# Kernel tuning notes

Hardware: AMD Instinct MI355X
Metric: run time of the kernel (lower is better)

The kernel has to match this reference:

```python
import jax, jax.numpy as jnp
import numpy as np

B, T, D = 16, 512, 256          # batch, seq_len, d_model (= num features = num graph nodes N)
H, MC, K, DE, DH = 4, 4, 3, 10, 128
GS, SS, AS = 4, 6, 4            # global/sector/asset regime states
TAU = 0.5
STEPS = 3                       # diffusion steps
HID = max(64, D)
DEC_H = max(64, D // 2)


def setup_inputs() -> dict:
    key = jax.random.key(0)
    ks = iter(jax.random.split(key, 64))

    def nrm(shape, s=0.02):
        return (s * jax.random.normal(next(ks), shape)).astype(jnp.float32)

    z = lambda *s: jnp.zeros(s, jnp.float32)
    o = lambda *s: jnp.ones(s, jnp.float32)
    p = dict(
        x=jax.random.normal(next(ks), (B, T, D), dtype=jnp.float32),
        # hierarchical regime controller
        gW1=nrm((D, HID)), gb1=z(HID), g_ln_w=o(HID), g_ln_b=z(HID),
        gW2=nrm((HID, GS)), gb2=z(GS),
        sW1=nrm((D, HID)), sb1=z(HID), sW2=nrm((HID, D * SS)), sb2=z(D * SS),
        aW1=nrm((D, HID)), ab1=z(HID), aW2=nrm((HID, D * AS)), ab2=z(D * AS),
        global_prior=z(GS), sector_prior=z(SS), asset_prior=z(AS),
        g2f=nrm((GS, D)),
        sector_emb=jax.random.normal(next(ks), (SS, D), dtype=jnp.float32),
        asset_emb=jax.random.normal(next(ks), (AS, D), dtype=jnp.float32),
        # bidirectional temporal scan (BI-Mamba stand-in)
        decay_f=nrm((D,), 1.0), decay_b=nrm((D,), 1.0),
        tW=nrm((D, D)), tb=z(D),
        # Bayesian MAGAC + diffusion graph prior
        psi=nrm((H, D, DE), 0.1), log_sigma=jnp.full((H,), -2.0, jnp.float32),
        step_logits=jnp.linspace(-1.0, 0.5, STEPS).astype(jnp.float32),
        noise_scale=jnp.full((STEPS,), 0.05, jnp.float32),
        Wk=nrm((K + 1, T, DH)),
        mean_w=nrm((DH,)), mean_b=z(), lv_w=nrm((DH,)), lv_b=z(),
        # risk-aware decoder
        dW1=nrm((D, DEC_H)), db1=z(DEC_H), d_ln_w=o(DEC_H), d_ln_b=z(DEC_H),
        mW=nrm((DEC_H,)), mb=z(), lvW=nrm((DEC_H,)), lvb=z(),
        cW=nrm((DEC_H,)), cb=z(),
    )
    return p


def _ln(h, w, b):
    m = h.mean(-1, keepdims=True)
    v = h.var(-1, keepdims=True)  # biased, matches torch LayerNorm
    return (h - m) / jnp.sqrt(v + 1e-5) * w + b


def _gelu(h):
    return jax.nn.gelu(h, approximate=False)


def _gumbel_softmax(k, logits):
    u = jax.random.uniform(k, logits.shape, minval=1e-6, maxval=1.0 - 1e-6)
    g = -jnp.log(-jnp.log(u))
    return jax.nn.softmax((logits + g) / TAU, axis=-1)


def _fwd(x, gW1, gb1, g_ln_w, g_ln_b, gW2, gb2, sW1, sb1, sW2, sb2,
         aW1, ab1, aW2, ab2, global_prior, sector_prior, asset_prior,
         g2f, sector_emb, asset_emb, decay_f, decay_b, tW, tb,
         psi, log_sigma, step_logits, noise_scale, Wk,
         mean_w, mean_b, lv_w, lv_b,
         dW1, db1, d_ln_w, d_ln_b, mW, mb, lvW, lvb, cW, cb):
    rk = jax.random.key(42)
    k_g, k_s, k_a, k_eps, k_diff = jax.random.split(rk, 5)

    # ---- hierarchical regime controller ----
    seq_mean = x.mean(1)                               # (B, D)
    diff_summary = (x[:, 1:] - x[:, :-1]).mean(1)      # (B, D)
    g_logits = _gelu(_ln(seq_mean @ gW1 + gb1, g_ln_w, g_ln_b)) @ gW2 + gb2
    s_logits = (_gelu(seq_mean @ sW1 + sb1) @ sW2 + sb2).reshape(B, D, SS)
    a_logits = (_gelu(diff_summary @ aW1 + ab1) @ aW2 + ab2).reshape(B, D, AS)
    g_probs = _gumbel_softmax(k_g, g_logits)
    s_probs = _gumbel_softmax(k_s, s_logits)
    a_probs = _gumbel_softmax(k_a, a_logits)
    global_gate = g_probs @ g2f                                   # (B, D)
    # diagonal of einsum('bfs,sd->bfd') == einsum('bfs,sf->bf')
    sector_gate = jnp.einsum('bfs,sf->bf', s_probs, sector_emb)
    asset_gate = jnp.einsum('bfs,sf->bf', a_probs, asset_emb)
    feature_gate = jax.nn.sigmoid(global_gate + sector_gate + asset_gate)
    gated_x = x * feature_gate[:, None, :]

    # ---- bidirectional temporal EMA scan (BI-Mamba stand-in) ----
    af = jax.nn.sigmoid(decay_f)
    abk = jax.nn.sigmoid(decay_b)
    xs = gated_x.transpose(1, 0, 2)                    # (T, B, D)

    def ema(a):
        def step(h, xt):
            h = a * h + (1.0 - a) * xt
            return h, h
        return step

    _, hf = jax.lax.scan(ema(af), jnp.zeros_like(xs[0]), xs)
    _, hb = jax.lax.scan(ema(abk), jnp.zeros_like(xs[0]), xs[::-1])
    temporal = (hf + hb[::-1]).transpose(1, 0, 2) @ tW + tb       # (B, T, D)
    node_major = temporal.transpose(0, 2, 1)                      # (B, N=D, T)

    # ---- Bayesian adjacency sampling (MC samples per head) ----
    logits = jnp.einsum('hne,hme->hnm', psi, psi) / jnp.sqrt(jnp.float32(DE))
    sigma = jnp.exp(log_sigma)                                    # (H,)
    eps = jax.random.normal(k_eps, (MC, H, D, D))
    A = jax.nn.softmax(logits[None] + sigma[None, :, None, None] * eps, axis=-1)

    # ---- diffusion refinement guided by regime features ----
    ctx = feature_gate.mean(0)
    ctx = ctx / (jnp.linalg.norm(ctx) + 1e-6)
    outer = ctx[:, None] * ctx[None, :]
    outer = outer / jnp.maximum(outer.sum(-1, keepdims=True), 1e-6)
    dkeys = jax.random.split(k_diff, STEPS)
    for s in range(STEPS):                             # fixed small loop, vectorized over (MC,H)
        alpha = jax.nn.sigmoid(step_logits[s])
        noise = noise_scale[s] * jax.random.normal(dkeys[s], A.shape)
        A = alpha * A + (1.0 - alpha) * outer + noise
        A = 0.5 * (A + jnp.swapaxes(A, -1, -2))
        A = jax.nn.softmax(A, axis=-1)

    # ---- K-hop graph conv, averaged over MC samples and heads ----
    Z = jnp.einsum('bnt,td->bnd', node_major, Wk[0])[None, None]  # hop 0
    P = jnp.broadcast_to(node_major, (MC, H, B, D, T))
    for k in range(1, K + 1):
        P = jnp.einsum('mhnp,mhbpt->mhbnt', A, P)
        Z = Z + jnp.einsum('mhbnt,td->mhbnd', P, Wk[k])
    Z = Z.mean((0, 1))                                            # (B, N, DH)
    graph_mean = Z @ mean_w + mean_b                              # (B, N)
    graph_logvar = Z @ lv_w + lv_b                                # (B, N)

    # ---- risk-aware decoder ----
    feat = _ln(_gelu(graph_mean @ dW1 + db1), d_ln_w, d_ln_b)     # (B, DEC_H)
    mean = feat @ mW + mb
    dec_logvar = feat @ lvW + lvb
    _cvar = jax.nn.sigmoid(feat @ cW + cb)  # auxiliary head (not in returned output)
    var = jnp.exp(dec_logvar) + jnp.exp(graph_logvar).sum(1)
    log_var = jnp.log(var)
    return jnp.stack([mean, log_var], axis=-1)                    # (B, 2)


def reference(x, gW1, gb1, g_ln_w, g_ln_b, gW2, gb2, sW1, sb1, sW2, sb2,
              aW1, ab1, aW2, ab2, global_prior, sector_prior, asset_prior,
              g2f, sector_emb, asset_emb, decay_f, decay_b, tW, tb,
              psi, log_sigma, step_logits, noise_scale, Wk,
              mean_w, mean_b, lv_w, lv_b,
              dW1, db1, d_ln_w, d_ln_b, mW, mb, lvW, lvb, cW, cb):
    return _fwd(x, gW1, gb1, g_ln_w, g_ln_b, gW2, gb2, sW1, sb1, sW2, sb2,
                aW1, ab1, aW2, ab2, global_prior, sector_prior, asset_prior,
                g2f, sector_emb, asset_emb, decay_f, decay_b, tW, tb,
                psi, log_sigma, step_logits, noise_scale, Wk,
                mean_w, mean_b, lv_w, lv_b,
                dW1, db1, d_ln_w, d_ln_b, mW, mb, lvW, lvb, cW, cb)
```

## Files before the change

### kernel.cpp

```cpp
#include <hip/hip_runtime.h>
#include <stdint.h>

#define PARTITIONABLE 1

namespace {

struct TFPair { uint32_t a, b; };

__host__ __device__ constexpr uint32_t rotl32(uint32_t x, int d) {
  return (x << d) | (x >> (32 - d));
}

__host__ __device__ constexpr TFPair tf2x32(uint32_t k0, uint32_t k1,
                                            uint32_t x0, uint32_t x1) {
  uint32_t k2 = k0 ^ k1 ^ 0x1BD11BDAu;
  x0 += k0; x1 += k1;
  x0 += x1; x1 = rotl32(x1, 13); x1 ^= x0;
  x0 += x1; x1 = rotl32(x1, 15); x1 ^= x0;
  x0 += x1; x1 = rotl32(x1, 26); x1 ^= x0;
  x0 += x1; x1 = rotl32(x1, 6);  x1 ^= x0;
  x0 += k1; x1 += k2 + 1u;
  x0 += x1; x1 = rotl32(x1, 17); x1 ^= x0;
  x0 += x1; x1 = rotl32(x1, 29); x1 ^= x0;
  x0 += x1; x1 = rotl32(x1, 16); x1 ^= x0;
  x0 += x1; x1 = rotl32(x1, 24); x1 ^= x0;
  x0 += k2; x1 += k0 + 2u;
  x0 += x1; x1 = rotl32(x1, 13); x1 ^= x0;
  x0 += x1; x1 = rotl32(x1, 15); x1 ^= x0;
  x0 += x1; x1 = rotl32(x1, 26); x1 ^= x0;
  x0 += x1; x1 = rotl32(x1, 6);  x1 ^= x0;
  x0 += k0; x1 += k1 + 3u;
  x0 += x1; x1 = rotl32(x1, 17); x1 ^= x0;
  x0 += x1; x1 = rotl32(x1, 29); x1 ^= x0;
  x0 += x1; x1 = rotl32(x1, 16); x1 ^= x0;
  x0 += x1; x1 = rotl32(x1, 24); x1 ^= x0;
  x0 += k1; x1 += k2 + 4u;
  x0 += x1; x1 = rotl32(x1, 13); x1 ^= x0;
  x0 += x1; x1 = rotl32(x1, 15); x1 ^= x0;
  x0 += x1; x1 = rotl32(x1, 26); x1 ^= x0;
  x0 += x1; x1 = rotl32(x1, 6);  x1 ^= x0;
  x0 += k2; x1 += k0 + 5u;
  return TFPair{x0, x1};
}

#if PARTITIONABLE
constexpr TFPair KG  = tf2x32(0u, 42u, 0u, 0u);
constexpr TFPair KS  = tf2x32(0u, 42u, 0u, 1u);
constexpr TFPair KA  = tf2x32(0u, 42u, 0u, 2u);
constexpr TFPair KE  = tf2x32(0u, 42u, 0u, 3u);
constexpr TFPair KD  = tf2x32(0u, 42u, 0u, 4u);
constexpr TFPair DK0 = tf2x32(KD.a, KD.b, 0u, 0u);
constexpr TFPair DK1 = tf2x32(KD.a, KD.b, 0u, 1u);
constexpr TFPair DK2 = tf2x32(KD.a, KD.b, 0u, 2u);
#else
constexpr TFPair SP0 = tf2x32(0u, 42u, 0u, 5u);
constexpr TFPair SP1 = tf2x32(0u, 42u, 1u, 6u);
constexpr TFPair SP2 = tf2x32(0u, 42u, 2u, 7u);
constexpr TFPair SP3 = tf2x32(0u, 42u, 3u, 8u);
constexpr TFPair SP4 = tf2x32(0u, 42u, 4u, 9u);
constexpr TFPair KG  = TFPair{SP0.a, SP1.a};
constexpr TFPair KS  = TFPair{SP2.a, SP3.a};
constexpr TFPair KA  = TFPair{SP4.a, SP0.b};
constexpr TFPair KE  = TFPair{SP1.b, SP2.b};
constexpr TFPair KD  = TFPair{SP3.b, SP4.b};
constexpr TFPair DP0 = tf2x32(KD.a, KD.b, 0u, 3u);
constexpr TFPair DP1 = tf2x32(KD.a, KD.b, 1u, 4u);
constexpr TFPair DP2 = tf2x32(KD.a, KD.b, 2u, 5u);
constexpr TFPair DK0 = TFPair{DP0.a, DP1.a};
constexpr TFPair DK1 = TFPair{DP2.a, DP0.b};
constexpr TFPair DK2 = TFPair{DP1.b, DP2.b};
#endif

__device__ __forceinline__ uint32_t rbits(uint32_t k0, uint32_t k1,
                                          uint32_t idx, uint32_t half) {
#if PARTITIONABLE
  TFPair t = tf2x32(k0, k1, 0u, idx);
  return t.a ^ t.b;
#else
  if (idx < half) return tf2x32(k0, k1, idx, idx + half).a;
  return tf2x32(k0, k1, idx - half, idx).b;
#endif
}

__device__ __forceinline__ float bits_to_u01(uint32_t bits) {
  return __uint_as_float((bits >> 9) | 0x3F800000u) - 1.0f;
}

__device__ __forceinline__ float gumbel_u(uint32_t k0, uint32_t k1,
                                          uint32_t idx, uint32_t half) {
  const float mn = 1e-6f;
  const float mx = 1.0f - 1e-6f;
  float f = bits_to_u01(rbits(k0, k1, idx, half));
  return fmaxf(mn, f * (mx - mn) + mn);
}

__device__ __forceinline__ float erfinv_f32(float x) {
  float w = -log1pf(-x * x);
  float p;
  if (w < 5.0f) {
    w -= 2.5f;
    p = 2.81022636e-08f;
    p = fmaf(p, w, 3.43273939e-07f);
    p = fmaf(p, w, -3.5233877e-06f);
    p = fmaf(p, w, -4.39150654e-06f);
    p = fmaf(p, w, 0.00021858087f);
    p = fmaf(p, w, -0.00125372503f);
    p = fmaf(p, w, -0.00417768164f);
    p = fmaf(p, w, 0.246640727f);
    p = fmaf(p, w, 1.50140941f);
  } else {
    w = sqrtf(w) - 3.0f;
    p = -0.000200214257f;
    p = fmaf(p, w, 0.000100950558f);
    p = fmaf(p, w, 0.00134934322f);
    p = fmaf(p, w, -0.00367342844f);
    p = fmaf(p, w, 0.00573950773f);
    p = fmaf(p, w, -0.0076224613f);
    p = fmaf(p, w, 0.00943887047f);
    p = fmaf(p, w, 1.00167406f);
    p = fmaf(p, w, 2.83297682f);
  }
  return p * x;
}

__device__ __forceinline__ float normal_from(uint32_t k0, uint32_t k1,
                                             uint32_t idx, uint32_t half) {
  const float lo = -0x1.fffffep-1f;
  float f = bits_to_u01(rbits(k0, k1, idx, half));
  float u = fmaxf(lo, f * 2.0f + lo);
  return 1.41421356237f * erfinv_f32(u);
}

__device__ __forceinline__ float gelu_f(float x) {
  return 0.5f * x * (1.0f + erff(x / 1.4142135623730951f));
}
__device__ __forceinline__ float sigmoid_f(float x) {
  return 1.0f / (1.0f + expf(-x));
}

__device__ __forceinline__ float wave_sum(float v) {
  #pragma unroll
  for (int m = 32; m > 0; m >>= 1) v += __shfl_xor(v, m);
  return v;
}
__device__ __forceinline__ float wave_max(float v) {
  #pragma unroll
  for (int m = 32; m > 0; m >>= 1) v = fmaxf(v, __shfl_xor(v, m));
  return v;
}
template <int NW>
__device__ __forceinline__ float blk_sum(float v, float* slots) {
  v = wave_sum(v);
  int wid = threadIdx.x >> 6;
  if ((threadIdx.x & 63) == 0) slots[wid] = v;
  __syncthreads();
  float r = slots[0];
  #pragma unroll
  for (int i = 1; i < NW; ++i) r += slots[i];
  return r;
}
template <int NW>
__device__ __forceinline__ float blk_max(float v, float* slots) {
  v = wave_max(v);
  int wid = threadIdx.x >> 6;
  if ((threadIdx.x & 63) == 0) slots[wid] = v;
  __syncthreads();
  float r = slots[0];
  #pragma unroll
  for (int i = 1; i < NW; ++i) r = fmaxf(r, slots[i]);
  return r;
}

struct Params {
  const float *x, *gW1, *gb1, *glnw, *glnb, *gW2, *gb2, *sW1, *sb1, *sW2, *sb2,
      *aW1, *ab1, *aW2, *ab2, *g2f, *semb, *aemb, *decay_f, *decay_b, *tW, *tb,
      *psi, *log_sigma, *step_logits, *noise_scale, *Wk, *mean_w, *mean_b,
      *lv_w, *lv_b, *dW1, *db1, *dlnw, *dlnb, *mW, *mb, *lvW, *lvb;
  float* out;
  float *ps, *ds, *fg, *ctx, *v, *sv, *u, *Pf, *Qf, *Pb, *Qb, *Lf, *Lb, *YH,
      *R1, *R2, *gm, *glv, *A, *A2, *nz;
};


__device__ __forceinline__ void phase_xsum(const Params& P, int bid, int tid) {
  int b = bid >> 4, tc = bid & 15;
  const float* xp = P.x + ((size_t)b * 512 + tc * 32) * 256 + tid;
  float s = 0.f;
  for (int i = 0; i < 32; ++i) s += xp[(size_t)i * 256];
  P.ps[(size_t)bid * 256 + tid] = s;
  if (tc == 0) {
    const float* xb = P.x + (size_t)b * 512 * 256 + tid;
    P.ds[b * 256 + tid] = (xb[(size_t)511 * 256] - xb[0]) / 511.0f;
  }
}

__device__ __forceinline__ void phase_ainit_row(const Params& P, float* smem,
                                                int blk, int tid) {
  float* pn = smem;
  float* s1 = smem + 12;
  float* s2 = smem + 16;
  int mh = blk >> 8, h = mh & 3, n = blk & 255, p = tid;
  if (p < 10) pn[p] = P.psi[(size_t)(h * 256 + n) * 10 + p];
  __syncthreads();
  const float* pp = P.psi + (size_t)(h * 256 + p) * 10;
  float s = 0.f;
  #pragma unroll
  for (int e = 0; e < 10; ++e) s = fmaf(pn[e], pp[e], s);
  float logit = s / sqrtf(10.0f);
  uint32_t idx = (uint32_t)blk * 256u + (uint32_t)p;
  float eps = normal_from(KE.a, KE.b, idx, 524288u);
  float val = logit + expf(P.log_sigma[h]) * eps;
  float mx = blk_max<4>(val, s1);
  float e = expf(val - mx);
  float sum = blk_sum<4>(e, s2);
  P.A[(size_t)blk * 256 + p] = e / sum;
}

__device__ __forceinline__ void phase_noise(const Params& P, int blk2,
                                            int tid) {
  const uint32_t dka[3] = {DK0.a, DK1.a, DK2.a};
  const uint32_t dkb[3] = {DK0.b, DK1.b, DK2.b};
  int s = blk2 >> 12;
  int row = blk2 & 4095;
  uint32_t e = (uint32_t)row * 256u + (uint32_t)tid;
  float z = normal_from(dka[s], dkb[s], e, 524288u);
  P.nz[(size_t)s * 1048576 + e] = P.noise_scale[s] * z;
}

__device__ __forceinline__ void phase_vcompute(const Params& P, int bid2,
                                               int tid) {
  int j = bid2 >> 2, tg = bid2 & 3;
  const float* wp = (j & 1) ? P.lv_w : P.mean_w;
  const float* Wkk = P.Wk + (size_t)(j >> 1) * 65536;
  int wid = tid >> 6, lane = tid & 63;
  float w0 = wp[lane], w1 = wp[64 + lane];
  for (int i = 0; i < 32; ++i) {
    int t = tg * 128 + wid * 32 + i;
    const float* row = Wkk + (size_t)t * 128;
    float s = row[lane] * w0 + row[64 + lane] * w1;
    s = wave_sum(s);
    if (lane == 0) P.v[j * 512 + t] = s;
  }
}

__device__ __forceinline__ void phase_svsum(const Params& P, float* smem,
                                            int tid) {
  float* slots = smem;
  #pragma unroll
  for (int j = 0; j < 8; ++j) {
    float val = P.v[j * 512 + tid] + P.v[j * 512 + 256 + tid];
    float s = blk_sum<4>(val, slots + 4 * j);
    if (tid == 0) P.sv[j] = s;
    __syncthreads();
  }
}

__device__ __forceinline__ void phase_hidden_gates(const Params& P,
                                                   float* smem, int bid,
                                                   int tid) {
  float* sms = smem;
  float* dss = smem + 256;
  float* hgG = smem + 512;
  float* hgS = smem + 768;
  float* hgA = smem + 1024;
  float* lvS = smem + 1280;
  float* lvA = smem + 1664;
  float* gsl = smem + 1920;
  float* gvals = smem + 1936;
  float* gpv = smem + 1940;
  float* s1 = smem + 1944;
  float* s2 = smem + 1948;
  int b = bid >> 2, f0 = (bid & 3) * 64;
  {
    float s = 0.f;
    for (int tc = 0; tc < 16; ++tc)
      s += P.ps[(size_t)(b * 16 + tc) * 256 + tid];
    sms[tid] = s / 512.0f;
    dss[tid] = P.ds[b * 256 + tid];
  }
  __syncthreads();
  {
    float h = P.gb1[tid];
    for (int d = 0; d < 256; ++d) h = fmaf(sms[d], P.gW1[d * 256 + tid], h);
    float mean = blk_sum<4>(h, s1) / 256.0f;
    float dv = h - mean;
    float var = blk_sum<4>(dv * dv, s2) / 256.0f;
    h = dv / sqrtf(var + 1e-5f) * P.glnw[tid] + P.glnb[tid];
    hgG[tid] = gelu_f(h);
    float h2 = P.sb1[tid];
    for (int d = 0; d < 256; ++d) h2 = fmaf(sms[d], P.sW1[d * 256 + tid], h2);
    hgS[tid] = gelu_f(h2);
    float h3 = P.ab1[tid];
    for (int d = 0; d < 256; ++d) h3 = fmaf(dss[d], P.aW1[d * 256 + tid], h3);
    hgA[tid] = gelu_f(h3);
  }
  __syncthreads();
  float lg[4];
  #pragma unroll
  for (int s = 0; s < 4; ++s)
    lg[s] = blk_sum<4>(hgG[tid] * P.gW2[tid * 4 + s], gsl + 4 * s);
  if (tid < 4) {
    float u = gumbel_u(KG.a, KG.b, (uint32_t)(b * 4 + tid), 32u);
    float g = -logf(-logf(u));
    gvals[tid] = (lg[tid] + P.gb2[tid] + g) / 0.5f;
  }
  __syncthreads();
  if (tid < 4) {
    float mx = fmaxf(fmaxf(gvals[0], gvals[1]), fmaxf(gvals[2], gvals[3]));
    float sum = expf(gvals[0] - mx) + expf(gvals[1] - mx) +
                expf(gvals[2] - mx) + expf(gvals[3] - mx);
    gpv[tid] = expf(gvals[tid] - mx) / sum;
  }
  {
    int o = tid;
    int fl = o / 6, s = o - fl * 6;
    int f = f0 + fl;
    const float* wp = P.sW2 + f * 6 + s;
    float acc = P.sb2[f * 6 + s];
    for (int d = 0; d < 256; ++d) acc = fmaf(hgS[d], wp[(size_t)d * 1536], acc);
    float u = gumbel_u(KS.a, KS.b, (uint32_t)(b * 256 + f) * 6u + s, 12288u);
    lvS[o] = (acc + (-logf(-logf(u)))) / 0.5f;
  }
  if (tid < 128) {
    int o = tid + 256;
    int fl = o / 6, s = o - fl * 6;
    int f = f0 + fl;
    const float* wp = P.sW2 + f * 6 + s;
    float acc = P.sb2[f * 6 + s];
    for (int d = 0; d < 256; ++d) acc = fmaf(hgS[d], wp[(size_t)d * 1536], acc);
    float u = gumbel_u(KS.a, KS.b, (uint32_t)(b * 256 + f) * 6u + s, 12288u);
    lvS[o] = (acc + (-logf(-logf(u)))) / 0.5f;
  }
  {
    int fl = tid >> 2, s = tid & 3;
    int f = f0 + fl;
    const float* wp = P.aW2 + f * 4 + s;
    float acc = P.ab2[f * 4 + s];
    for (int d = 0; d < 256; ++d) acc = fmaf(hgA[d], wp[(size_t)d * 1024], acc);
    float u = gumbel_u(KA.a, KA.b, (uint32_t)(b * 256 + f) * 4u + s, 8192u);
    lvA[tid] = (acc + (-logf(-logf(u)))) / 0.5f;
  }
  __syncthreads();
  if (tid < 64) {
    int f = f0 + tid;
    float v0 = lvS[tid * 6 + 0], v1 = lvS[tid * 6 + 1], v2 = lvS[tid * 6 + 2];
    float v3 = lvS[tid * 6 + 3], v4 = lvS[tid * 6 + 4], v5 = lvS[tid * 6 + 5];
    float mx = fmaxf(fmaxf(fmaxf(v0, v1), fmaxf(v2, v3)), fmaxf(v4, v5));
    float e0 = expf(v0 - mx), e1 = expf(v1 - mx), e2 = expf(v2 - mx);
    float e3 = expf(v3 - mx), e4 = expf(v4 - mx), e5 = expf(v5 - mx);
    float ssum = e0 + e1 + e2 + e3 + e4 + e5;
    float sg = (e0 / ssum) * P.semb[0 * 256 + f] + (e1 / ssum) * P.semb[1 * 256 + f] +
               (e2 / ssum) * P.semb[2 * 256 + f] + (e3 / ssum) * P.semb[3 * 256 + f] +
               (e4 / ssum) * P.semb[4 * 256 + f] + (e5 / ssum) * P.semb[5 * 256 + f];
    float a0 = lvA[tid * 4 + 0], a1 = lvA[tid * 4 + 1];
    float a2 = lvA[tid * 4 + 2], a3 = lvA[tid * 4 + 3];
    float amx = fmaxf(fmaxf(a0, a1), fmaxf(a2, a3));
    float x0 = expf(a0 - amx), x1 = expf(a1 - amx);
    float x2 = expf(a2 - amx), x3 = expf(a3 - amx);
    float asum = x0 + x1 + x2 + x3;
    float ag = (x0 / asum) * P.aemb[0 * 256 + f] + (x1 / asum) * P.aemb[1 * 256 + f] +
               (x2 / asum) * P.aemb[2 * 256 + f] + (x3 / asum) * P.aemb[3 * 256 + f];
    float gg = 0.f;
    #pragma unroll
    for (int s = 0; s < 4; ++s) gg = fmaf(gpv[s], P.g2f[s * 256 + f], gg);
    P.fg[b * 256 + f] = sigmoid_f(gg + sg + ag);
  }
}

__device__ __forceinline__ void phase_scan1(const Params& P, float* smem,
                                            int ch, int tid) {
  float* vv = smem;
  int b = ch >> 4, c = ch & 15;
  int d = tid;
  vv[(d >> 5) * 32 + (d & 31)] = P.v[(d >> 5) * 512 + c * 32 + (d & 31)];
  __syncthreads();
  float af = sigmoid_f(P.decay_f[d]);
  float ab = sigmoid_f(P.decay_b[d]);
  float r_x[32];
  const float* xp = P.x + ((size_t)b * 512 + c * 32) * 256 + d;
  #pragma unroll
  for (int i = 0; i < 32; ++i) r_x[i] = xp[(size_t)i * 256];
  float h = 0.f, pw = 1.f;
  float Pr[8], Q[8];
  #pragma unroll
  for (int j = 0; j < 8; ++j) { Pr[j] = 0.f; Q[j] = 0.f; }
  #pragma unroll
  for (int i = 0; i < 32; ++i) {
    h = fmaf(af, h, (1.0f - af) * r_x[i]);
    pw *= af;
    #pragma unroll
    for (int j = 0; j < 8; ++j) {
      float vj = vv[j * 32 + i];
      Pr[j] = fmaf(h, vj, Pr[j]);
      Q[j] = fmaf(pw, vj, Q[j]);
    }
  }
  size_t base = ((size_t)(b * 16 + c) * 8) * 256 + d;
  #pragma unroll
  for (int j = 0; j < 8; ++j) {
    P.Pf[base + j * 256] = Pr[j];
    P.Qf[base + j * 256] = Q[j];
  }
  P.Lf[(b * 16 + c) * 256 + d] = h;
  h = 0.f; pw = 1.f;
  #pragma unroll
  for (int j = 0; j < 8; ++j) { Pr[j] = 0.f; Q[j] = 0.f; }
  #pragma unroll
  for (int i = 31; i >= 0; --i) {
    h = fmaf(ab, h, (1.0f - ab) * r_x[i]);
    pw *= ab;
    #pragma unroll
    for (int j = 0; j < 8; ++j) {
      float vj = vv[j * 32 + i];
      Pr[j] = fmaf(h, vj, Pr[j]);
      Q[j] = fmaf(pw, vj, Q[j]);
    }
  }
  #pragma unroll
  for (int j = 0; j < 8; ++j) {
    P.Pb[base + j * 256] = Pr[j];
    P.Qb[base + j * 256] = Q[j];
  }
  P.Lb[(b * 16 + c) * 256 + d] = h;
}

__device__ __forceinline__ void phase_scan2(const Params& P, int blk, int tid) {
  int b = blk >> 3, j = blk & 7;
  int d = tid;
  float af = sigmoid_f(P.decay_f[d]);
  float ab = sigmoid_f(P.decay_b[d]);
  float af32 = af, ab32 = ab;
  #pragma unroll
  for (int q = 0; q < 5; ++q) { af32 *= af32; ab32 *= ab32; }
  float acc = 0.f, H = 0.f;
  for (int c = 0; c < 16; ++c) {
    size_t base = ((size_t)(b * 16 + c) * 8 + j) * 256 + d;
    acc += P.Pf[base] + H * P.Qf[base];
    H = P.Lf[(b * 16 + c) * 256 + d] + af32 * H;
  }
  H = 0.f;
  for (int c = 15; c >= 0; --c) {
    size_t base = ((size_t)(b * 16 + c) * 8 + j) * 256 + d;
    acc += P.Pb[base] + H * P.Qb[base];
    H = P.Lb[(b * 16 + c) * 256 + d] + ab32 * H;
  }
  P.u[(b * 8 + j) * 256 + d] = acc;
}

__device__ __forceinline__ void phase_ctx(const Params& P, float* smem,
                                          int tid) {
  float* s1 = smem;
  float* s2 = smem + 4;
  float c = 0.f;
  for (int b = 0; b < 16; ++b) c += P.fg[b * 256 + tid];
  c /= 16.0f;
  float ss = blk_sum<4>(c * c, s1);
  float cv = c / (sqrtf(ss) + 1e-6f);
  P.ctx[tid] = cv;
  float S = blk_sum<4>(cv, s2);
  if (tid == 0) P.ctx[256] = S;
}

__device__ __forceinline__ void phase_ygemm(const Params& P, float* smem,
                                            int blk32, int tid) {
  float* As = smem;
  float* Bs = smem + 1056;
  float* svs = smem + 2112;
  int n0 = (blk32 & 7) * 32, m0 = (blk32 >> 3) * 32;
  int tx = tid & 31, ty = tid >> 5;
  if (tid < 8) svs[tid] = P.sv[tid];
  float acc[4] = {0.f, 0.f, 0.f, 0.f};
  for (int k0 = 0; k0 < 256; k0 += 32) {
    #pragma unroll
    for (int l = 0; l < 4; ++l) {
      int e = tid + l * 256, r = e >> 5, cc = e & 31;
      int row = m0 + r;
      As[r * 33 + cc] = P.u[(size_t)row * 256 + k0 + cc] *
                        P.fg[(row >> 3) * 256 + k0 + cc];
      Bs[r * 33 + cc] = P.tW[(size_t)(k0 + r) * 256 + n0 + cc];
    }
    __syncthreads();
    #pragma unroll
    for (int kk = 0; kk < 32; ++kk) {
      float bv = Bs[kk * 33 + tx];
      #pragma unroll
      for (int i = 0; i < 4; ++i)
        acc[i] = fmaf(As[(ty + 8 * i) * 33 + kk], bv, acc[i]);
    }
    __syncthreads();
  }
  int n = n0 + tx;
  float tbn = P.tb[n];
  float mb0 = P.mean_b[0], lb0 = P.lv_b[0];
  #pragma unroll
  for (int i = 0; i < 4; ++i) {
    int row = m0 + ty + 8 * i;
    int b = row >> 3, j = row & 7;
    float val = acc[i] + tbn * svs[j];
    if (j == 0) P.gm[b * 256 + n] = val + mb0;
    else if (j == 1) P.glv[b * 256 + n] = val + lb0;
    else {
      int k = (j >> 1) - 1, proj = j & 1;
      P.YH[k * 8192 + n * 32 + b * 2 + proj] = val;
    }
  }
}

__device__ __forceinline__ void phase_mix_row(const Params& P, float* smem,
                                              int sidx, const float* Ain,
                                              float* Aout, int blk, int tid) {
  float* s1 = smem;
  float* s2 = smem + 4;
  float alpha = sigmoid_f(P.step_logits[sidx]);
  float S = P.ctx[256];
  float cp = P.ctx[tid];
  int mh = blk >> 8, n = blk & 255, p = tid;
  float cn = P.ctx[n];
  float o_np = (cn * cp) / fmaxf(cn * S, 1e-6f);
  float o_pn = (cp * cn) / fmaxf(cp * S, 1e-6f);
  const float* nzs = P.nz + (size_t)sidx * 1048576;
  float nz_np = nzs[(size_t)blk * 256 + p];
  float nz_pn = nzs[(size_t)mh * 65536 + (size_t)p * 256 + n];
  float a_np = Ain[(size_t)mh * 65536 + n * 256 + p];
  float a_pn = Ain[(size_t)mh * 65536 + p * 256 + n];
  float m_np = alpha * a_np + (1.0f - alpha) * o_np + nz_np;
  float m_pn = alpha * a_pn + (1.0f - alpha) * o_pn + nz_pn;
  float val = 0.5f * (m_np + m_pn);
  float mx = blk_max<4>(val, s1);
  float e = expf(val - mx);
  float sum = blk_sum<4>(e, s2);
  Aout[(size_t)blk * 256 + p] = e / sum;
}

__device__ __forceinline__ void phase_horner(const Params& P, float* smem,
                                             const float* A, const float* Rin,
                                             int sRin, const float* Yadd,
                                             float* Rout, int bid, int tid) {
  float* As = smem;
  float* Bs = smem + 1056;
  int nt = bid & 7, mh = bid >> 3;
  int n0 = nt * 32;
  int tx = tid & 31, ty = tid >> 5;
  float acc[4] = {0.f, 0.f, 0.f, 0.f};
  const float* Ab = A + (size_t)mh * 65536;
  const float* Rb = Rin + (size_t)mh * sRin;
  for (int k0 = 0; k0 < 256; k0 += 32) {
    #pragma unroll
    for (int l = 0; l < 4; ++l) {
      int e = tid + l * 256, r = e >> 5, cc = e & 31;
      As[r * 33 + cc] = Ab[(size_t)(n0 + r) * 256 + k0 + cc];
      Bs[r * 33 + cc] = Rb[(size_t)(k0 + r) * 32 + cc];
    }
    __syncthreads();
    #pragma unroll
    for (int kk = 0; kk < 32; ++kk) {
      float bv = Bs[kk * 33 + tx];
      #pragma unroll
      for (int i = 0; i < 4; ++i)
        acc[i] = fmaf(As[(ty + 8 * i) * 33 + kk], bv, acc[i]);
    }
    __syncthreads();
  }
  #pragma unroll
  for (int i = 0; i < 4; ++i) {
    int n = n0 + ty + 8 * i;
    float vv = acc[i];
    if (Yadd) vv += Yadd[n * 32 + tx];
    Rout[(size_t)mh * 8192 + (size_t)n * 32 + tx] = vv;
  }
}

__device__ __forceinline__ void phase_horner_final(const Params& P,
                                                   float* smem, int bid,
                                                   int tid) {
  float* As = smem;
  float* Bs = smem + 1056;
  int nt = bid & 7, mh = bid >> 3;
  int n0 = nt * 32;
  int tx = tid & 31, ty = tid >> 5;
  float acc[4] = {0.f, 0.f, 0.f, 0.f};
  const float* Ab = P.A2 + (size_t)mh * 65536;
  const float* Rb = P.R2 + (size_t)mh * 8192;
  for (int k0 = 0; k0 < 256; k0 += 32) {
    #pragma unroll
    for (int l = 0; l < 4; ++l) {
      int e = tid + l * 256, r = e >> 5, cc = e & 31;
      As[r * 33 + cc] = Ab[(size_t)(n0 + r) * 256 + k0 + cc];
      Bs[r * 33 + cc] = Rb[(size_t)(k0 + r) * 32 + cc];
    }
    __syncthreads();
    #pragma unroll
    for (int kk = 0; kk < 32; ++kk) {
      float bv = Bs[kk * 33 + tx];
      #pragma unroll
      for (int i = 0; i < 4; ++i)
        acc[i] = fmaf(As[(ty + 8 * i) * 33 + kk], bv, acc[i]);
    }
    __syncthreads();
  }
  int bb = tx >> 1, proj = tx & 1;
  float* dst = proj ? P.glv : P.gm;
  #pragma unroll
  for (int i = 0; i < 4; ++i) {
    int n = n0 + ty + 8 * i;
    atomicAdd(dst + bb * 256 + n, acc[i] * 0.0625f);
  }
}

__device__ __forceinline__ void phase_findec(const Params& P, float* smem,
                                             int bid, int tid) {
  float* gmv = smem;
  float* sl = smem + 256;
  int b = bid;
  float gmn = P.gm[b * 256 + tid];
  float gln = P.glv[b * 256 + tid];
  gmv[tid] = gmn;
  float se = expf(gln);
  __syncthreads();
  float sumexp = blk_sum<4>(se, sl);
  float h = 0.f;
  if (tid < 128) {
    h = P.db1[tid];
    for (int n = 0; n < 256; ++n) h = fmaf(gmv[n], P.dW1[n * 128 + tid], h);
    h = gelu_f(h);
  }
  float mean = blk_sum<4>(tid < 128 ? h : 0.f, sl + 4) / 128.0f;
  float dv = (tid < 128) ? h - mean : 0.f;
  float var = blk_sum<4>(dv * dv, sl + 8) / 128.0f;
  float feat = (tid < 128) ? dv / sqrtf(var + 1e-5f) * P.dlnw[tid] + P.dlnb[tid]
                           : 0.f;
  float m_c = blk_sum<4>(tid < 128 ? feat * P.mW[tid] : 0.f, sl + 12) + P.mb[0];
  float lv_c = blk_sum<4>(tid < 128 ? feat * P.lvW[tid] : 0.f, sl + 16) + P.lvb[0];
  if (tid == 0) {
    P.out[b * 2 + 0] = m_c;
    P.out[b * 2 + 1] = logf(expf(lv_c) + sumexp);
  }
}


__global__ __launch_bounds__(256) void kN0(Params P) {
  __shared__ float smem[20];
  int bid = blockIdx.x, tid = threadIdx.x;
  if (bid < 256) phase_xsum(P, bid, tid);
  else if (bid < 4352) phase_ainit_row(P, smem, bid - 256, tid);
  else if (bid < 16640) phase_noise(P, bid - 4352, tid);
  else phase_vcompute(P, bid - 16640, tid);
}

__global__ __launch_bounds__(256) void kN1(Params P) {
  __shared__ float smem[1952];
  int bid = blockIdx.x, tid = threadIdx.x;
  if (bid < 64) phase_hidden_gates(P, smem, bid, tid);
  else if (bid < 320) phase_scan1(P, smem, bid - 64, tid);
  else phase_svsum(P, smem, tid);
}

__global__ __launch_bounds__(256) void kN2(Params P) {
  __shared__ float smem[8];
  int bid = blockIdx.x, tid = threadIdx.x;
  if (bid < 128) phase_scan2(P, bid, tid);
  else phase_ctx(P, smem, tid);
}

__global__ __launch_bounds__(256) void kM0(Params P) {
  __shared__ float smem[2120];
  int bid = blockIdx.x, tid = threadIdx.x;
  if (bid < 4096) phase_mix_row(P, smem, 0, P.A, P.A2, bid, tid);
  else phase_ygemm(P, smem, bid - 4096, tid);
}
__global__ __launch_bounds__(256) void kM1(Params P) {
  __shared__ float smem[8];
  phase_mix_row(P, smem, 1, P.A2, P.A, blockIdx.x, threadIdx.x);
}
__global__ __launch_bounds__(256) void kM2(Params P) {
  __shared__ float smem[8];
  phase_mix_row(P, smem, 2, P.A, P.A2, blockIdx.x, threadIdx.x);
}

__global__ __launch_bounds__(256) void kH1(Params P) {
  __shared__ float smem[2112];
  phase_horner(P, smem, P.A2, P.YH + 2 * 8192, 0, P.YH + 8192, P.R1,
               blockIdx.x, threadIdx.x);
}
__global__ __launch_bounds__(256) void kH2(Params P) {
  __shared__ float smem[2112];
  phase_horner(P, smem, P.A2, P.R1, 8192, P.YH, P.R2, blockIdx.x, threadIdx.x);
}
__global__ __launch_bounds__(256) void kH3(Params P) {
  __shared__ float smem[2112];
  phase_horner_final(P, smem, blockIdx.x, threadIdx.x);
}

__global__ __launch_bounds__(256) void kFin(Params P) {
  __shared__ float smem[276];
  phase_findec(P, smem, blockIdx.x, threadIdx.x);
}

constexpr size_t O_PS = 0;
constexpr size_t O_DS = 65536;
constexpr size_t O_FG = 69632;
constexpr size_t O_CTX = 73728;
constexpr size_t O_V = 74048;
constexpr size_t O_SV = 78144;
constexpr size_t O_U = 78208;
constexpr size_t O_PF = 110976;
constexpr size_t O_QF = 635264;
constexpr size_t O_PB = 1159552;
constexpr size_t O_QB = 1683840;
constexpr size_t O_LF = 2208128;
constexpr size_t O_LB = 2273664;
constexpr size_t O_YH = 2339200;
constexpr size_t O_R1 = 2363776;
constexpr size_t O_R2 = 2494848;
constexpr size_t O_GM = 2625920;
constexpr size_t O_GLV = 2630016;
constexpr size_t O_A = 2634112;
constexpr size_t O_A2 = 3682688;
constexpr size_t O_NZ = 4731264;

}

extern "C" void kernel_launch(void* const* d_in, const int* in_sizes, int n_in,
                              void* d_out, int out_size, void* d_ws,
                              size_t ws_size, hipStream_t stream) {
  (void)in_sizes; (void)n_in; (void)out_size; (void)ws_size;
  float* w = (float*)d_ws;
  Params prm;
  prm.x = (const float*)d_in[0];
  prm.gW1 = (const float*)d_in[1];
  prm.gb1 = (const float*)d_in[2];
  prm.glnw = (const float*)d_in[3];
  prm.glnb = (const float*)d_in[4];
  prm.gW2 = (const float*)d_in[5];
  prm.gb2 = (const float*)d_in[6];
  prm.sW1 = (const float*)d_in[7];
  prm.sb1 = (const float*)d_in[8];
  prm.sW2 = (const float*)d_in[9];
  prm.sb2 = (const float*)d_in[10];
  prm.aW1 = (const float*)d_in[11];
  prm.ab1 = (const float*)d_in[12];
  prm.aW2 = (const float*)d_in[13];
  prm.ab2 = (const float*)d_in[14];
  prm.g2f = (const float*)d_in[18];
  prm.semb = (const float*)d_in[19];
  prm.aemb = (const float*)d_in[20];
  prm.decay_f = (const float*)d_in[21];
  prm.decay_b = (const float*)d_in[22];
  prm.tW = (const float*)d_in[23];
  prm.tb = (const float*)d_in[24];
  prm.psi = (const float*)d_in[25];
  prm.log_sigma = (const float*)d_in[26];
  prm.step_logits = (const float*)d_in[27];
  prm.noise_scale = (const float*)d_in[28];
  prm.Wk = (const float*)d_in[29];
  prm.mean_w = (const float*)d_in[30];
  prm.mean_b = (const float*)d_in[31];
  prm.lv_w = (const float*)d_in[32];
  prm.lv_b = (const float*)d_in[33];
  prm.dW1 = (const float*)d_in[34];
  prm.db1 = (const float*)d_in[35];
  prm.dlnw = (const float*)d_in[36];
  prm.dlnb = (const float*)d_in[37];
  prm.mW = (const float*)d_in[38];
  prm.mb = (const float*)d_in[39];
  prm.lvW = (const float*)d_in[40];
  prm.lvb = (const float*)d_in[41];
  prm.out = (float*)d_out;
  prm.ps = w + O_PS;
  prm.ds = w + O_DS;
  prm.fg = w + O_FG;
  prm.ctx = w + O_CTX;
  prm.v = w + O_V;
  prm.sv = w + O_SV;
  prm.u = w + O_U;
  prm.Pf = w + O_PF;
  prm.Qf = w + O_QF;
  prm.Pb = w + O_PB;
  prm.Qb = w + O_QB;
  prm.Lf = w + O_LF;
  prm.Lb = w + O_LB;
  prm.YH = w + O_YH;
  prm.R1 = w + O_R1;
  prm.R2 = w + O_R2;
  prm.gm = w + O_GM;
  prm.glv = w + O_GLV;
  prm.A = w + O_A;
  prm.A2 = w + O_A2;
  prm.nz = w + O_NZ;

  kN0<<<16672, 256, 0, stream>>>(prm);
  kN1<<<321, 256, 0, stream>>>(prm);
  kN2<<<129, 256, 0, stream>>>(prm);
  kM0<<<4128, 256, 0, stream>>>(prm);
  kM1<<<4096, 256, 0, stream>>>(prm);
  kM2<<<4096, 256, 0, stream>>>(prm);
  kH1<<<128, 256, 0, stream>>>(prm);
  kH2<<<128, 256, 0, stream>>>(prm);
  kH3<<<128, 256, 0, stream>>>(prm);
  kFin<<<16, 256, 0, stream>>>(prm);
}
```

Before: 344.3 us.

## Split hidden-layer GEMVs from gate computation and rebalance kernel stages

The first-layer controller GEMVs move out of the per-(batch, feature-quarter) gate blocks into a separate phase with one block per (head, batch). Each hidden vector is now computed once instead of four times, and the work is spread over 48 blocks instead of being serialized inside 64. The gate logic moves to the next kernel and reads the hidden vectors from workspace. ygemm and ctx move to a new small kernel, so kM0 becomes a pure mix kernel, at the cost of one extra launch and extra workspace traffic.

```diff
diff --git a/kernel.cpp b/kernel.cpp
--- a/kernel.cpp
+++ b/kernel.cpp
@@ -177,8 +177,8 @@
       *psi, *log_sigma, *step_logits, *noise_scale, *Wk, *mean_w, *mean_b,
       *lv_w, *lv_b, *dW1, *db1, *dlnw, *dlnb, *mW, *mb, *lvW, *lvb;
   float* out;
-  float *ps, *ds, *fg, *ctx, *v, *sv, *u, *Pf, *Qf, *Pb, *Qb, *Lf, *Lb, *YH,
-      *R1, *R2, *gm, *glv, *A, *A2, *nz;
+  float *ps, *ds, *hgG, *hgS, *hgA, *fg, *ctx, *v, *sv, *u, *Pf, *Qf, *Pb,
+      *Qb, *Lf, *Lb, *YH, *R1, *R2, *gm, *glv, *A, *A2, *nz;
 };
 
 
@@ -243,6 +243,37 @@
   }
 }
 
+__device__ __forceinline__ void phase_hidden(const Params& P, float* smem,
+                                             int bid, int tid) {
+  float* inv = smem;
+  float* s1 = smem + 256;
+  float* s2 = smem + 260;
+  int head = bid >> 4, b = bid & 15;
+  float iv;
+  if (head < 2) {
+    float s = 0.f;
+    for (int tc = 0; tc < 16; ++tc)
+      s += P.ps[(size_t)(b * 16 + tc) * 256 + tid];
+    iv = s / 512.0f;
+  } else {
+    iv = P.ds[b * 256 + tid];
+  }
+  inv[tid] = iv;
+  __syncthreads();
+  const float* W1 = (head == 0) ? P.gW1 : (head == 1) ? P.sW1 : P.aW1;
+  const float* b1 = (head == 0) ? P.gb1 : (head == 1) ? P.sb1 : P.ab1;
+  float h = b1[tid];
+  for (int d = 0; d < 256; ++d) h = fmaf(inv[d], W1[d * 256 + tid], h);
+  if (head == 0) {
+    float mean = blk_sum<4>(h, s1) / 256.0f;
+    float dv = h - mean;
+    float var = blk_sum<4>(dv * dv, s2) / 256.0f;
+    h = dv / sqrtf(var + 1e-5f) * P.glnw[tid] + P.glnb[tid];
+  }
+  float* outp = (head == 0) ? P.hgG : (head == 1) ? P.hgS : P.hgA;
+  outp[b * 256 + tid] = gelu_f(h);
+}
+
 __device__ __forceinline__ void phase_svsum(const Params& P, float* smem,
                                             int tid) {
   float* slots = smem;
@@ -255,50 +286,25 @@
   }
 }
 
-__device__ __forceinline__ void phase_hidden_gates(const Params& P,
-                                                   float* smem, int bid,
-                                                   int tid) {
-  float* sms = smem;
-  float* dss = smem + 256;
-  float* hgG = smem + 512;
-  float* hgS = smem + 768;
-  float* hgA = smem + 1024;
-  float* lvS = smem + 1280;
-  float* lvA = smem + 1664;
-  float* gsl = smem + 1920;
-  float* gvals = smem + 1936;
-  float* gpv = smem + 1940;
-  float* s1 = smem + 1944;
-  float* s2 = smem + 1948;
+__device__ __forceinline__ void phase_gates(const Params& P, float* smem,
+                                            int bid, int tid) {
+  float* hgGs = smem;
+  float* hgSs = smem + 256;
+  float* hgAs = smem + 512;
+  float* lvS = smem + 768;
+  float* lvA = smem + 1152;
+  float* gsl = smem + 1408;
+  float* gvals = smem + 1424;
+  float* gpv = smem + 1428;
   int b = bid >> 2, f0 = (bid & 3) * 64;
-  {
-    float s = 0.f;
-    for (int tc = 0; tc < 16; ++tc)
-      s += P.ps[(size_t)(b * 16 + tc) * 256 + tid];
-    sms[tid] = s / 512.0f;
-    dss[tid] = P.ds[b * 256 + tid];
-  }
-  __syncthreads();
-  {
-    float h = P.gb1[tid];
-    for (int d = 0; d < 256; ++d) h = fmaf(sms[d], P.gW1[d * 256 + tid], h);
-    float mean = blk_sum<4>(h, s1) / 256.0f;
-    float dv = h - mean;
-    float var = blk_sum<4>(dv * dv, s2) / 256.0f;
-    h = dv / sqrtf(var + 1e-5f) * P.glnw[tid] + P.glnb[tid];
-    hgG[tid] = gelu_f(h);
-    float h2 = P.sb1[tid];
-    for (int d = 0; d < 256; ++d) h2 = fmaf(sms[d], P.sW1[d * 256 + tid], h2);
-    hgS[tid] = gelu_f(h2);
-    float h3 = P.ab1[tid];
-    for (int d = 0; d < 256; ++d) h3 = fmaf(dss[d], P.aW1[d * 256 + tid], h3);
-    hgA[tid] = gelu_f(h3);
-  }
+  hgGs[tid] = P.hgG[b * 256 + tid];
+  hgSs[tid] = P.hgS[b * 256 + tid];
+  hgAs[tid] = P.hgA[b * 256 + tid];
   __syncthreads();
   float lg[4];
   #pragma unroll
   for (int s = 0; s < 4; ++s)
-    lg[s] = blk_sum<4>(hgG[tid] * P.gW2[tid * 4 + s], gsl + 4 * s);
+    lg[s] = blk_sum<4>(hgGs[tid] * P.gW2[tid * 4 + s], gsl + 4 * s);
   if (tid < 4) {
     float u = gumbel_u(KG.a, KG.b, (uint32_t)(b * 4 + tid), 32u);
     float g = -logf(-logf(u));
@@ -317,7 +323,7 @@
     int f = f0 + fl;
     const float* wp = P.sW2 + f * 6 + s;
     float acc = P.sb2[f * 6 + s];
-    for (int d = 0; d < 256; ++d) acc = fmaf(hgS[d], wp[(size_t)d * 1536], acc);
+    for (int d = 0; d < 256; ++d) acc = fmaf(hgSs[d], wp[(size_t)d * 1536], acc);
     float u = gumbel_u(KS.a, KS.b, (uint32_t)(b * 256 + f) * 6u + s, 12288u);
     lvS[o] = (acc + (-logf(-logf(u)))) / 0.5f;
   }
@@ -327,7 +333,7 @@
     int f = f0 + fl;
     const float* wp = P.sW2 + f * 6 + s;
     float acc = P.sb2[f * 6 + s];
-    for (int d = 0; d < 256; ++d) acc = fmaf(hgS[d], wp[(size_t)d * 1536], acc);
+    for (int d = 0; d < 256; ++d) acc = fmaf(hgSs[d], wp[(size_t)d * 1536], acc);
     float u = gumbel_u(KS.a, KS.b, (uint32_t)(b * 256 + f) * 6u + s, 12288u);
     lvS[o] = (acc + (-logf(-logf(u)))) / 0.5f;
   }
@@ -336,7 +342,7 @@
     int f = f0 + fl;
     const float* wp = P.aW2 + f * 4 + s;
     float acc = P.ab2[f * 4 + s];
-    for (int d = 0; d < 256; ++d) acc = fmaf(hgA[d], wp[(size_t)d * 1024], acc);
+    for (int d = 0; d < 256; ++d) acc = fmaf(hgAs[d], wp[(size_t)d * 1024], acc);
     float u = gumbel_u(KA.a, KA.b, (uint32_t)(b * 256 + f) * 4u + s, 8192u);
     lvA[tid] = (acc + (-logf(-logf(u)))) / 0.5f;
   }
@@ -648,25 +654,30 @@
 }
 
 __global__ __launch_bounds__(256) void kN1(Params P) {
-  __shared__ float smem[1952];
+  __shared__ float smem[264];
   int bid = blockIdx.x, tid = threadIdx.x;
-  if (bid < 64) phase_hidden_gates(P, smem, bid, tid);
-  else if (bid < 320) phase_scan1(P, smem, bid - 64, tid);
+  if (bid < 48) phase_hidden(P, smem, bid, tid);
+  else if (bid < 304) phase_scan1(P, smem, bid - 48, tid);
   else phase_svsum(P, smem, tid);
 }
 
 __global__ __launch_bounds__(256) void kN2(Params P) {
-  __shared__ float smem[8];
+  __shared__ float smem[1440];
   int bid = blockIdx.x, tid = threadIdx.x;
-  if (bid < 128) phase_scan2(P, bid, tid);
-  else phase_ctx(P, smem, tid);
-}
-
-__global__ __launch_bounds__(256) void kM0(Params P) {
+  if (bid < 64) phase_gates(P, smem, bid, tid);
+  else phase_scan2(P, bid - 64, tid);
+}
+
+__global__ __launch_bounds__(256) void kN3(Params P) {
   __shared__ float smem[2120];
   int bid = blockIdx.x, tid = threadIdx.x;
-  if (bid < 4096) phase_mix_row(P, smem, 0, P.A, P.A2, bid, tid);
-  else phase_ygemm(P, smem, bid - 4096, tid);
+  if (bid < 32) phase_ygemm(P, smem, bid, tid);
+  else phase_ctx(P, smem, tid);
+}
+
+__global__ __launch_bounds__(256) void kM0(Params P) {
+  __shared__ float smem[8];
+  phase_mix_row(P, smem, 0, P.A, P.A2, blockIdx.x, threadIdx.x);
 }
 __global__ __launch_bounds__(256) void kM1(Params P) {
   __shared__ float smem[8];
@@ -698,25 +709,28 @@
 
 constexpr size_t O_PS = 0;
 constexpr size_t O_DS = 65536;
-constexpr size_t O_FG = 69632;
-constexpr size_t O_CTX = 73728;
-constexpr size_t O_V = 74048;
-constexpr size_t O_SV = 78144;
-constexpr size_t O_U = 78208;
-constexpr size_t O_PF = 110976;
-constexpr size_t O_QF = 635264;
-constexpr size_t O_PB = 1159552;
-constexpr size_t O_QB = 1683840;
-constexpr size_t O_LF = 2208128;
-constexpr size_t O_LB = 2273664;
-constexpr size_t O_YH = 2339200;
-constexpr size_t O_R1 = 2363776;
-constexpr size_t O_R2 = 2494848;
-constexpr size_t O_GM = 2625920;
-constexpr size_t O_GLV = 2630016;
-constexpr size_t O_A = 2634112;
-constexpr size_t O_A2 = 3682688;
-constexpr size_t O_NZ = 4731264;
+constexpr size_t O_HGG = 69632;
+constexpr size_t O_HGS = 73728;
+constexpr size_t O_HGA = 77824;
+constexpr size_t O_FG = 81920;
+constexpr size_t O_CTX = 86016;
+constexpr size_t O_V = 86336;
+constexpr size_t O_SV = 90432;
+constexpr size_t O_U = 90496;
+constexpr size_t O_PF = 123264;
+constexpr size_t O_QF = 647552;
+constexpr size_t O_PB = 1171840;
+constexpr size_t O_QB = 1696128;
+constexpr size_t O_LF = 2220416;
+constexpr size_t O_LB = 2285952;
+constexpr size_t O_YH = 2351488;
+constexpr size_t O_R1 = 2376064;
+constexpr size_t O_R2 = 2507136;
+constexpr size_t O_GM = 2638208;
+constexpr size_t O_GLV = 2642304;
+constexpr size_t O_A = 2646400;
+constexpr size_t O_A2 = 3694976;
+constexpr size_t O_NZ = 4743552;
 
 }
 
@@ -768,6 +782,9 @@
   prm.out = (float*)d_out;
   prm.ps = w + O_PS;
   prm.ds = w + O_DS;
+  prm.hgG = w + O_HGG;
+  prm.hgS = w + O_HGS;
+  prm.hgA = w + O_HGA;
   prm.fg = w + O_FG;
   prm.ctx = w + O_CTX;
   prm.v = w + O_V;
@@ -789,9 +806,10 @@
   prm.nz = w + O_NZ;
 
   kN0<<<16672, 256, 0, stream>>>(prm);
-  kN1<<<321, 256, 0, stream>>>(prm);
-  kN2<<<129, 256, 0, stream>>>(prm);
-  kM0<<<4128, 256, 0, stream>>>(prm);
+  kN1<<<305, 256, 0, stream>>>(prm);
+  kN2<<<192, 256, 0, stream>>>(prm);
+  kN3<<<33, 256, 0, stream>>>(prm);
+  kM0<<<4096, 256, 0, stream>>>(prm);
   kM1<<<4096, 256, 0, stream>>>(prm);
   kM2<<<4096, 256, 0, stream>>>(prm);
   kH1<<<128, 256, 0, stream>>>(prm);
```

After: 332.5 us. 3.4% less time.
